# Optimization experiments

Hardware: AMD Instinct MI355X
Metric: run time of the kernel (lower is better)

## Reference

```python
import jax, jax.numpy as jnp
import numpy as np

N, E, F_IN, H, O = 50000, 800000, 128, 64, 1


def _gcn_conv(x, row, col, ew, W, b, n_nodes):
    """PyG GCNConv: add self-loops (weight 1), symmetric deg normalization,
    linear transform (no bias inside lin), scatter-add aggregation, then +bias."""
    loop = jnp.arange(n_nodes, dtype=row.dtype)
    r = jnp.concatenate([row, loop])
    c = jnp.concatenate([col, loop])
    w = jnp.concatenate([ew, jnp.ones((n_nodes,), dtype=ew.dtype)])
    deg = jax.ops.segment_sum(w, c, num_segments=n_nodes)            # [N]
    dis = jnp.where(deg > 0, jax.lax.rsqrt(jnp.maximum(deg, 1e-12)), 0.0)
    norm = dis[r] * w * dis[c]                                       # [E+N]
    h = x @ W                                                        # [N, out]
    msg = h[r] * norm[:, None]                                       # gather + scale
    agg = jax.ops.segment_sum(msg, c, num_segments=n_nodes)          # scatter-add
    return agg + b


def setup_inputs() -> dict:
    key = jax.random.key(0)
    ks = jax.random.split(key, 14)
    s = 0.02
    return {
        "x": jax.random.normal(ks[0], (N, F_IN), dtype=jnp.float32),
        "edge_index": jax.random.randint(ks[1], (2, E), 0, N, dtype=jnp.int64),
        "edge_weight": jax.random.uniform(ks[2], (E,), dtype=jnp.float32),
        "W1": jax.random.normal(ks[3], (F_IN, H), dtype=jnp.float32) * s,
        "b1": jnp.zeros((H,), dtype=jnp.float32),
        "W2": jax.random.normal(ks[4], (H, H), dtype=jnp.float32) * s,
        "b2": jnp.zeros((H,), dtype=jnp.float32),
        "W_ih": jax.random.normal(ks[5], (4 * H, H), dtype=jnp.float32) * s,
        "W_hh": jax.random.normal(ks[6], (4 * H, H), dtype=jnp.float32) * s,
        "b_ih": jax.random.normal(ks[7], (4 * H,), dtype=jnp.float32) * s,
        "b_hh": jax.random.normal(ks[8], (4 * H,), dtype=jnp.float32) * s,
        "W_reg": jax.random.normal(ks[9], (H, O), dtype=jnp.float32) * s,
        "b_reg": jnp.zeros((O,), dtype=jnp.float32),
    }


def reference(x, edge_index, edge_weight, W1, b1, W2, b2,
              W_ih, W_hh, b_ih, b_hh, W_reg, b_reg):
    row, col = edge_index[0], edge_index[1]
    n = x.shape[0]
    h = jax.nn.relu(_gcn_conv(x, row, col, edge_weight, W1, b1, n))
    h = jax.nn.relu(_gcn_conv(h, row, col, edge_weight, W2, b2, n))
    # single-step LSTM, zero initial (h0, c0); PyTorch gate order i, f, g, o
    hd = W_ih.shape[1]
    h0 = jnp.zeros((n, hd), dtype=h.dtype)
    gates = h @ W_ih.T + h0 @ W_hh.T + b_ih + b_hh                   # [N, 4H]
    i, f, g, o = jnp.split(gates, 4, axis=-1)
    c = jax.nn.sigmoid(f) * 0.0 + jax.nn.sigmoid(i) * jnp.tanh(g)    # c0 = 0
    hn = jax.nn.sigmoid(o) * jnp.tanh(c)                             # lstm_out[:, -1]
    return hn @ W_reg + b_reg
```

## Files before the change

kernel.cpp:

```cpp
#include <hip/hip_runtime.h>
#include <math.h>


#define QN 6272
#define NOCT 8
#define NPAD (NOCT * QN)
#define NSLICE 128
#define HIST_BLOCKS (NSLICE * NOCT)

__device__ __forceinline__ float sigmoidf_(float x) {
    return 1.0f / (1.0f + expf(-x));
}

__global__ __launch_bounds__(256) void hist_gemm1_k(
        const int* __restrict__ col, unsigned short* __restrict__ part,
        int E, int N,
        const float* __restrict__ x, const float* __restrict__ W1,
        float* __restrict__ C) {
    extern __shared__ char smem[];
    const int t = threadIdx.x;
    if (blockIdx.x < HIST_BLOCKS) {
        int* hc = (int*)smem;
        const int s = blockIdx.x >> 3;
        const int q = blockIdx.x & 7;
        const int lo = q * QN;
        for (int i = t; i < QN; i += 256) hc[i] = 0;
        __syncthreads();
        const int per = (E + NSLICE - 1) / NSLICE;
        const int e0 = s * per, e1 = min(E, e0 + per);
        int e = e0 + t;
        for (; e + 768 < e1; e += 1024) {
            int c0 = col[e], c1 = col[e + 256], c2 = col[e + 512], c3 = col[e + 768];
            unsigned r0 = (unsigned)(c0 - lo), r1 = (unsigned)(c1 - lo);
            unsigned r2 = (unsigned)(c2 - lo), r3 = (unsigned)(c3 - lo);
            if (r0 < (unsigned)QN && (unsigned)c0 < (unsigned)N) atomicAdd(&hc[r0], 1);
            if (r1 < (unsigned)QN && (unsigned)c1 < (unsigned)N) atomicAdd(&hc[r1], 1);
            if (r2 < (unsigned)QN && (unsigned)c2 < (unsigned)N) atomicAdd(&hc[r2], 1);
            if (r3 < (unsigned)QN && (unsigned)c3 < (unsigned)N) atomicAdd(&hc[r3], 1);
        }
        for (; e < e1; e += 256) {
            int c = col[e];
            unsigned rel = (unsigned)(c - lo);
            if (rel < (unsigned)QN && (unsigned)c < (unsigned)N) atomicAdd(&hc[rel], 1);
        }
        __syncthreads();
        unsigned short* dst = part + (size_t)s * NPAD + lo;
        for (int i = t; i < QN; i += 256) dst[i] = (unsigned short)hc[i];
    } else {
        float (*xs)[68] = (float (*)[68])smem;
        float* ws = (float*)(smem + 64 * 68 * sizeof(float));
        const int n0 = (int)(blockIdx.x - HIST_BLOCKS) * 64;
        for (int base = t * 4; base < 128 * 64; base += 1024)
            *(float4*)(ws + base) = *(const float4*)(W1 + base);
        const int cg = t & 15, ng = t >> 4;
        const int colj = cg * 4, nb = ng * 4;
        float acc[4][4];
#pragma unroll
        for (int i = 0; i < 4; ++i)
#pragma unroll
            for (int j = 0; j < 4; ++j) acc[i][j] = 0.0f;
        for (int k0 = 0; k0 < 128; k0 += 64) {
            __syncthreads();
            for (int base = t * 4; base < 64 * 64; base += 1024) {
                int r = base >> 6, k = base & 63;
                int node = n0 + r;
                float4 v = make_float4(0.f, 0.f, 0.f, 0.f);
                if (node < N) v = *(const float4*)(x + (size_t)node * 128 + k0 + k);
                *(float4*)&xs[r][k] = v;
            }
            __syncthreads();
#pragma unroll 4
            for (int kk = 0; kk < 64; kk += 4) {
                float4 a[4];
#pragma unroll
                for (int i = 0; i < 4; ++i) a[i] = *(float4*)&xs[nb + i][kk];
#pragma unroll
                for (int j = 0; j < 4; ++j) {
                    float4 bv = *(float4*)&ws[(size_t)(k0 + kk + j) * 64 + colj];
                    float av[4];
                    switch (j) {
                        case 0: av[0]=a[0].x; av[1]=a[1].x; av[2]=a[2].x; av[3]=a[3].x; break;
                        case 1: av[0]=a[0].y; av[1]=a[1].y; av[2]=a[2].y; av[3]=a[3].y; break;
                        case 2: av[0]=a[0].z; av[1]=a[1].z; av[2]=a[2].z; av[3]=a[3].z; break;
                        default:av[0]=a[0].w; av[1]=a[1].w; av[2]=a[2].w; av[3]=a[3].w; break;
                    }
#pragma unroll
                    for (int i = 0; i < 4; ++i) {
                        acc[i][0] = fmaf(av[i], bv.x, acc[i][0]);
                        acc[i][1] = fmaf(av[i], bv.y, acc[i][1]);
                        acc[i][2] = fmaf(av[i], bv.z, acc[i][2]);
                        acc[i][3] = fmaf(av[i], bv.w, acc[i][3]);
                    }
                }
            }
        }
#pragma unroll
        for (int i = 0; i < 4; ++i) {
            int node = n0 + nb + i;
            if (node < N)
                *(float4*)(C + (size_t)node * 64 + colj) =
                    make_float4(acc[i][0], acc[i][1], acc[i][2], acc[i][3]);
        }
    }
}

__global__ __launch_bounds__(256) void prefixA_k(const unsigned short* __restrict__ part,
                                                 unsigned short* __restrict__ coff,
                                                 int* __restrict__ cnt,
                                                 int* __restrict__ bsum) {
    __shared__ int r[256];
    const int t = threadIdx.x;
    const int i = blockIdx.x * 256 + t;
    int acc = 0;
    for (int s = 0; s < NSLICE; ++s) {
        size_t idx = (size_t)s * NPAD + i;
        coff[idx] = (unsigned short)acc;
        acc += part[idx];
    }
    cnt[i] = acc;
    r[t] = acc;
    __syncthreads();
#pragma unroll
    for (int off = 128; off > 0; off >>= 1) {
        if (t < off) r[t] += r[t + off];
        __syncthreads();
    }
    if (t == 0) bsum[blockIdx.x] = r[0];
}

__global__ __launch_bounds__(256) void scanBC_k(const int* __restrict__ cnt,
                                                const int* __restrict__ bsum,
                                                int* __restrict__ rowptr, int NBLK) {
    __shared__ int s[2][256];
    __shared__ int red[256];
    const int t = threadIdx.x, b = blockIdx.x;
    const int i = b * 256 + t;
    int v = cnt[i];
    int pin = 0;
    s[0][t] = v;
    __syncthreads();
#pragma unroll
    for (int off = 1; off < 256; off <<= 1) {
        int xo = s[pin][t];
        if (t >= off) xo += s[pin][t - off];
        s[pin ^ 1][t] = xo;
        pin ^= 1;
        __syncthreads();
    }
    int excl = s[pin][t] - v;
    red[t] = (t < b && t < NBLK) ? bsum[t] : 0;
    __syncthreads();
#pragma unroll
    for (int off = 128; off > 0; off >>= 1) {
        if (t < off) red[t] += red[t + off];
        __syncthreads();
    }
    rowptr[i] = excl + red[0];
}

__global__ __launch_bounds__(256) void fill_k(const int* __restrict__ row,
                                              const int* __restrict__ col,
                                              const float* __restrict__ ew,
                                              const int* __restrict__ rowptr,
                                              const unsigned short* __restrict__ coff,
                                              int2* __restrict__ pairs, int E, int N) {
    __shared__ int lcur[QN];
    const int t = threadIdx.x;
    const int s = blockIdx.x >> 3;
    const int q = blockIdx.x & 7;
    const int lo = q * QN;
    const unsigned short* cof = coff + (size_t)s * NPAD + lo;
    const int* rp = rowptr + lo;
    for (int i = t; i < QN; i += 256) lcur[i] = rp[i] + (int)cof[i];
    __syncthreads();
    const int per = (E + NSLICE - 1) / NSLICE;
    const int e0 = s * per, e1 = min(E, e0 + per);
    int e = e0 + t;
    for (; e + 768 < e1; e += 1024) {
        int c0 = col[e], c1 = col[e + 256], c2 = col[e + 512], c3 = col[e + 768];
        unsigned r0 = (unsigned)(c0 - lo), r1 = (unsigned)(c1 - lo);
        unsigned r2 = (unsigned)(c2 - lo), r3 = (unsigned)(c3 - lo);
        if (r0 < (unsigned)QN && (unsigned)c0 < (unsigned)N) {
            int r = row[e]; float w = ew[e];
            if ((unsigned)r >= (unsigned)N) { r = 0; w = 0.0f; }
            pairs[atomicAdd(&lcur[r0], 1)] = make_int2(r, __float_as_int(w));
        }
        if (r1 < (unsigned)QN && (unsigned)c1 < (unsigned)N) {
            int r = row[e + 256]; float w = ew[e + 256];
            if ((unsigned)r >= (unsigned)N) { r = 0; w = 0.0f; }
            pairs[atomicAdd(&lcur[r1], 1)] = make_int2(r, __float_as_int(w));
        }
        if (r2 < (unsigned)QN && (unsigned)c2 < (unsigned)N) {
            int r = row[e + 512]; float w = ew[e + 512];
            if ((unsigned)r >= (unsigned)N) { r = 0; w = 0.0f; }
            pairs[atomicAdd(&lcur[r2], 1)] = make_int2(r, __float_as_int(w));
        }
        if (r3 < (unsigned)QN && (unsigned)c3 < (unsigned)N) {
            int r = row[e + 768]; float w = ew[e + 768];
            if ((unsigned)r >= (unsigned)N) { r = 0; w = 0.0f; }
            pairs[atomicAdd(&lcur[r3], 1)] = make_int2(r, __float_as_int(w));
        }
    }
    for (; e < e1; e += 256) {
        int c = col[e];
        unsigned rel = (unsigned)(c - lo);
        if (rel < (unsigned)QN && (unsigned)c < (unsigned)N) {
            int r = row[e]; float w = ew[e];
            if ((unsigned)r >= (unsigned)N) { r = 0; w = 0.0f; }
            pairs[atomicAdd(&lcur[rel], 1)] = make_int2(r, __float_as_int(w));
        }
    }
}

__global__ __launch_bounds__(256) void degsum_k(const int* __restrict__ rowptr,
                                                const int2* __restrict__ pairs,
                                                float* __restrict__ dis, int N) {
    int i = blockIdx.x * 256 + threadIdx.x;
    if (i >= N) return;
    int b = rowptr[i], en = rowptr[i + 1];
    float s = 0.0f;
    for (int e = b; e < en; ++e) s += __int_as_float(pairs[e].y);
    dis[i] = rsqrtf(s + 1.0f);
}

__global__ __launch_bounds__(256) void aggregate_k(const float* __restrict__ h,
                                                   const int* __restrict__ rowptr,
                                                   const int2* __restrict__ pairs,
                                                   const float* __restrict__ dis,
                                                   const float* __restrict__ bias,
                                                   float* __restrict__ out, int N) {
    const int t = threadIdx.x;
    const int lane = t & 63;
    const int n0 = (blockIdx.x * 4 + (t >> 6)) * 4;
    if (n0 >= N) return;

    int rp[5];
#pragma unroll
    for (int k = 0; k < 5; ++k) rp[k] = rowptr[min(n0 + k, N)];
    const int beg = rp[0], end = rp[4];

    float acc[4] = {0.f, 0.f, 0.f, 0.f};
    for (int base = beg; base < end; base += 64) {
        const int m = min(64, end - base);
        int ps = 0; float pv = 0.0f;
        if (lane < m) {
            int2 p = pairs[base + lane];
            ps = p.x;
            pv = __int_as_float(p.y) * dis[p.x];
        }
        const unsigned pu = __float_as_uint(pv);
#pragma unroll
        for (int i = 0; i < 4; ++i) {
            const int s0 = max(rp[i] - base, 0);
            const int s1 = min(rp[i + 1] - base, m);
            int jj = s0;
            for (; jj + 8 <= s1; jj += 8) {
                int a0 = __builtin_amdgcn_readlane(ps, jj);
                int a1 = __builtin_amdgcn_readlane(ps, jj + 1);
                int a2 = __builtin_amdgcn_readlane(ps, jj + 2);
                int a3 = __builtin_amdgcn_readlane(ps, jj + 3);
                int a4 = __builtin_amdgcn_readlane(ps, jj + 4);
                int a5 = __builtin_amdgcn_readlane(ps, jj + 5);
                int a6 = __builtin_amdgcn_readlane(ps, jj + 6);
                int a7 = __builtin_amdgcn_readlane(ps, jj + 7);
                float v0 = __uint_as_float(__builtin_amdgcn_readlane(pu, jj));
                float v1 = __uint_as_float(__builtin_amdgcn_readlane(pu, jj + 1));
                float v2 = __uint_as_float(__builtin_amdgcn_readlane(pu, jj + 2));
                float v3 = __uint_as_float(__builtin_amdgcn_readlane(pu, jj + 3));
                float v4 = __uint_as_float(__builtin_amdgcn_readlane(pu, jj + 4));
                float v5 = __uint_as_float(__builtin_amdgcn_readlane(pu, jj + 5));
                float v6 = __uint_as_float(__builtin_amdgcn_readlane(pu, jj + 6));
                float v7 = __uint_as_float(__builtin_amdgcn_readlane(pu, jj + 7));
                float h0 = h[(size_t)a0 * 64 + lane];
                float h1 = h[(size_t)a1 * 64 + lane];
                float h2 = h[(size_t)a2 * 64 + lane];
                float h3 = h[(size_t)a3 * 64 + lane];
                float h4 = h[(size_t)a4 * 64 + lane];
                float h5 = h[(size_t)a5 * 64 + lane];
                float h6 = h[(size_t)a6 * 64 + lane];
                float h7 = h[(size_t)a7 * 64 + lane];
                acc[i] = fmaf(h0, v0, acc[i]);
                acc[i] = fmaf(h1, v1, acc[i]);
                acc[i] = fmaf(h2, v2, acc[i]);
                acc[i] = fmaf(h3, v3, acc[i]);
                acc[i] = fmaf(h4, v4, acc[i]);
                acc[i] = fmaf(h5, v5, acc[i]);
                acc[i] = fmaf(h6, v6, acc[i]);
                acc[i] = fmaf(h7, v7, acc[i]);
            }
            for (; jj + 4 <= s1; jj += 4) {
                int a0 = __builtin_amdgcn_readlane(ps, jj);
                int a1 = __builtin_amdgcn_readlane(ps, jj + 1);
                int a2 = __builtin_amdgcn_readlane(ps, jj + 2);
                int a3 = __builtin_amdgcn_readlane(ps, jj + 3);
                float v0 = __uint_as_float(__builtin_amdgcn_readlane(pu, jj));
                float v1 = __uint_as_float(__builtin_amdgcn_readlane(pu, jj + 1));
                float v2 = __uint_as_float(__builtin_amdgcn_readlane(pu, jj + 2));
                float v3 = __uint_as_float(__builtin_amdgcn_readlane(pu, jj + 3));
                float h0 = h[(size_t)a0 * 64 + lane];
                float h1 = h[(size_t)a1 * 64 + lane];
                float h2 = h[(size_t)a2 * 64 + lane];
                float h3 = h[(size_t)a3 * 64 + lane];
                acc[i] = fmaf(h0, v0, acc[i]);
                acc[i] = fmaf(h1, v1, acc[i]);
                acc[i] = fmaf(h2, v2, acc[i]);
                acc[i] = fmaf(h3, v3, acc[i]);
            }
            for (; jj < s1; ++jj) {
                int   a0 = __builtin_amdgcn_readlane(ps, jj);
                float v0 = __uint_as_float(__builtin_amdgcn_readlane(pu, jj));
                acc[i] = fmaf(h[(size_t)a0 * 64 + lane], v0, acc[i]);
            }
        }
    }
#pragma unroll
    for (int i = 0; i < 4; ++i) {
        int node = n0 + i;
        if (node < N) {
            float d = dis[node];
            float a = acc[i];
            a = fmaf(d, h[(size_t)node * 64 + lane], a);
            a = fmaf(d, a, bias[lane]);
            out[(size_t)node * 64 + lane] = fmaxf(a, 0.0f);
        }
    }
}

template <int K>
__global__ __launch_bounds__(256) void gemm64_k(const float* __restrict__ A,
                                                const float* __restrict__ W,
                                                float* __restrict__ C, int M) {
    __shared__ float xs[64][68];
    __shared__ float ws[K][64];
    const int t  = threadIdx.x;
    const int n0 = blockIdx.x * 64;

    for (int base = t * 4; base < K * 64; base += 1024)
        *(float4*)((float*)ws + base) = *(const float4*)(W + base);

    const int cg = t & 15, ng = t >> 4;
    const int col = cg * 4, nb = ng * 4;
    float acc[4][4];
#pragma unroll
    for (int i = 0; i < 4; ++i)
#pragma unroll
        for (int j = 0; j < 4; ++j) acc[i][j] = 0.0f;

    for (int k0 = 0; k0 < K; k0 += 64) {
        __syncthreads();
        for (int base = t * 4; base < 64 * 64; base += 1024) {
            int r = base >> 6, k = base & 63;
            int node = n0 + r;
            float4 v = make_float4(0.f, 0.f, 0.f, 0.f);
            if (node < M) v = *(const float4*)(A + (size_t)node * K + k0 + k);
            *(float4*)&xs[r][k] = v;
        }
        __syncthreads();
#pragma unroll 4
        for (int kk = 0; kk < 64; kk += 4) {
            float4 a[4];
#pragma unroll
            for (int i = 0; i < 4; ++i) a[i] = *(float4*)&xs[nb + i][kk];
#pragma unroll
            for (int j = 0; j < 4; ++j) {
                float4 bv = *(float4*)&ws[k0 + kk + j][col];
                float av[4];
                switch (j) {
                    case 0: av[0]=a[0].x; av[1]=a[1].x; av[2]=a[2].x; av[3]=a[3].x; break;
                    case 1: av[0]=a[0].y; av[1]=a[1].y; av[2]=a[2].y; av[3]=a[3].y; break;
                    case 2: av[0]=a[0].z; av[1]=a[1].z; av[2]=a[2].z; av[3]=a[3].z; break;
                    default:av[0]=a[0].w; av[1]=a[1].w; av[2]=a[2].w; av[3]=a[3].w; break;
                }
#pragma unroll
                for (int i = 0; i < 4; ++i) {
                    acc[i][0] = fmaf(av[i], bv.x, acc[i][0]);
                    acc[i][1] = fmaf(av[i], bv.y, acc[i][1]);
                    acc[i][2] = fmaf(av[i], bv.z, acc[i][2]);
                    acc[i][3] = fmaf(av[i], bv.w, acc[i][3]);
                }
            }
        }
    }
#pragma unroll
    for (int i = 0; i < 4; ++i) {
        int node = n0 + nb + i;
        if (node < M)
            *(float4*)(C + (size_t)node * 64 + col) =
                make_float4(acc[i][0], acc[i][1], acc[i][2], acc[i][3]);
    }
}

__global__ __launch_bounds__(256) void lstm_head_k(const float* __restrict__ h,
                                                   const float* __restrict__ Wih,
                                                   const float* __restrict__ bih,
                                                   const float* __restrict__ bhh,
                                                   const float* __restrict__ Wreg,
                                                   const float* __restrict__ breg,
                                                   float* __restrict__ out, int N) {
    __shared__ float wt[64 * 192];
    __shared__ float hsT[64 * 64];
    const int t = threadIdx.x;
    const int n0 = blockIdx.x * 64;

    {
        const int j = t & 63, kq = (t >> 6) * 4;
#pragma unroll
        for (int gid = 0; gid < 3; ++gid) {
            const int gBase = (gid == 0) ? 0 : (gid == 1 ? 128 : 192);
            const int gOff = gid * 64;
#pragma unroll
            for (int it = 0; it < 4; ++it) {
                int k0 = it * 16 + kq;
                float4 w = *(const float4*)(Wih + (size_t)(gBase + j) * 64 + k0);
                wt[(k0 + 0) * 192 + gOff + j] = w.x;
                wt[(k0 + 1) * 192 + gOff + j] = w.y;
                wt[(k0 + 2) * 192 + gOff + j] = w.z;
                wt[(k0 + 3) * 192 + gOff + j] = w.w;
            }
        }
    }
    {
        const int r = t & 63, kq = (t >> 6) * 4;
        const int node = n0 + r;
#pragma unroll
        for (int it = 0; it < 4; ++it) {
            int k0 = it * 16 + kq;
            float4 v = make_float4(0.f, 0.f, 0.f, 0.f);
            if (node < N) v = *(const float4*)(h + (size_t)node * 64 + k0);
            hsT[(k0 + 0) * 64 + r] = v.x;
            hsT[(k0 + 1) * 64 + r] = v.y;
            hsT[(k0 + 2) * 64 + r] = v.z;
            hsT[(k0 + 3) * 64 + r] = v.w;
        }
    }

    const int cg = t & 15, ng = t >> 4;
    const int col = cg * 4, nb = ng * 4;
    float4 bi4 = *(const float4*)(bih + col);
    float4 bg4 = *(const float4*)(bih + 128 + col);
    float4 bo4 = *(const float4*)(bih + 192 + col);
    {
        float4 h0 = *(const float4*)(bhh + col);
        float4 h1 = *(const float4*)(bhh + 128 + col);
        float4 h2 = *(const float4*)(bhh + 192 + col);
        bi4.x += h0.x; bi4.y += h0.y; bi4.z += h0.z; bi4.w += h0.w;
        bg4.x += h1.x; bg4.y += h1.y; bg4.z += h1.z; bg4.w += h1.w;
        bo4.x += h2.x; bo4.y += h2.y; bo4.z += h2.z; bo4.w += h2.w;
    }
    float4 wr4 = *(const float4*)(Wreg + col);
    const float br = breg[0];

    __syncthreads();

    float ai[4][4], ag[4][4], ao[4][4];
#pragma unroll
    for (int i = 0; i < 4; ++i)
#pragma unroll
        for (int j = 0; j < 4; ++j) { ai[i][j] = 0.f; ag[i][j] = 0.f; ao[i][j] = 0.f; }

#pragma unroll 4
    for (int k = 0; k < 64; ++k) {
        float4 a  = *(float4*)&hsT[k * 64 + nb];
        float4 wi = *(float4*)&wt[k * 192 + col];
        float4 wg = *(float4*)&wt[k * 192 + 64 + col];
        float4 wo = *(float4*)&wt[k * 192 + 128 + col];
        const float av[4] = {a.x, a.y, a.z, a.w};
#pragma unroll
        for (int i = 0; i < 4; ++i) {
            ai[i][0] = fmaf(av[i], wi.x, ai[i][0]);
            ai[i][1] = fmaf(av[i], wi.y, ai[i][1]);
            ai[i][2] = fmaf(av[i], wi.z, ai[i][2]);
            ai[i][3] = fmaf(av[i], wi.w, ai[i][3]);
            ag[i][0] = fmaf(av[i], wg.x, ag[i][0]);
            ag[i][1] = fmaf(av[i], wg.y, ag[i][1]);
            ag[i][2] = fmaf(av[i], wg.z, ag[i][2]);
            ag[i][3] = fmaf(av[i], wg.w, ag[i][3]);
            ao[i][0] = fmaf(av[i], wo.x, ao[i][0]);
            ao[i][1] = fmaf(av[i], wo.y, ao[i][1]);
            ao[i][2] = fmaf(av[i], wo.z, ao[i][2]);
            ao[i][3] = fmaf(av[i], wo.w, ao[i][3]);
        }
    }

    const float bia[4] = {bi4.x, bi4.y, bi4.z, bi4.w};
    const float bga[4] = {bg4.x, bg4.y, bg4.z, bg4.w};
    const float boa[4] = {bo4.x, bo4.y, bo4.z, bo4.w};
    const float wra[4] = {wr4.x, wr4.y, wr4.z, wr4.w};
    float res[4];
#pragma unroll
    for (int i = 0; i < 4; ++i) {
        float s = 0.f;
#pragma unroll
        for (int j = 0; j < 4; ++j) {
            float gi = ai[i][j] + bia[j];
            float gg = ag[i][j] + bga[j];
            float go = ao[i][j] + boa[j];
            float cc = sigmoidf_(gi) * tanhf(gg);
            float hn = sigmoidf_(go) * tanhf(cc);
            s = fmaf(hn, wra[j], s);
        }
        res[i] = s;
    }
#pragma unroll
    for (int off = 8; off > 0; off >>= 1) {
#pragma unroll
        for (int i = 0; i < 4; ++i) res[i] += __shfl_down(res[i], off);
    }
    if (cg == 0) {
#pragma unroll
        for (int i = 0; i < 4; ++i) {
            int node = n0 + nb + i;
            if (node < N) out[node] = res[i] + br;
        }
    }
}

extern "C" void kernel_launch(void* const* d_in, const int* in_sizes, int n_in,
                              void* d_out, int out_size, void* d_ws, size_t ws_size,
                              hipStream_t stream) {
    const float* x    = (const float*)d_in[0];
    const int*   ei   = (const int*)d_in[1];
    const float* ew   = (const float*)d_in[2];
    const float* W1   = (const float*)d_in[3];
    const float* b1   = (const float*)d_in[4];
    const float* W2   = (const float*)d_in[5];
    const float* b2   = (const float*)d_in[6];
    const float* Wih  = (const float*)d_in[7];
    const float* bih  = (const float*)d_in[9];
    const float* bhh  = (const float*)d_in[10];
    const float* Wreg = (const float*)d_in[11];
    const float* breg = (const float*)d_in[12];
    float* out = (float*)d_out;

    const int N = out_size;
    const int E = in_sizes[1] / 2;
    const int* row = ei;
    const int* col = ei + E;

    const int NB   = (N + 255) / 256;
    const int NBLK = NPAD / 256;

    char* wsb = (char*)d_ws;
    size_t off = 0;
    unsigned short* part = (unsigned short*)(wsb + off); off += (size_t)NSLICE * NPAD * 2;
    unsigned short* coff = (unsigned short*)(wsb + off); off += (size_t)NSLICE * NPAD * 2;
    float* bufA   = (float*)(wsb + off); off += (size_t)N * 64 * 4;
    float* bufB   = (float*)(wsb + off); off += (size_t)N * 64 * 4;
    float* bufC   = (float*)(wsb + off); off += (size_t)N * 64 * 4;
    int2*  pairs  = (int2*) (wsb + off); off += (size_t)E * 8;
    float* dis    = (float*)(wsb + off); off += (size_t)NPAD * 4;
    int*   cnt    = (int*)  (wsb + off); off += (size_t)NPAD * 4;
    int*   rowptr = (int*)  (wsb + off); off += ((size_t)NPAD + 64) * 4;
    int*   bsum   = (int*)  (wsb + off); off += 1024;

    const int gb = (N + 63) / 64;
    const int ab = (N + 15) / 16;
    const size_t DSM = 64 * 68 * sizeof(float) + 128 * 64 * sizeof(float);

    hist_gemm1_k<<<HIST_BLOCKS + gb, 256, DSM, stream>>>(col, part, E, N, x, W1, bufA);
    prefixA_k<<<NBLK, 256, 0, stream>>>(part, coff, cnt, bsum);
    scanBC_k<<<NBLK, 256, 0, stream>>>(cnt, bsum, rowptr, NBLK);
    fill_k<<<HIST_BLOCKS, 256, 0, stream>>>(row, col, ew, rowptr, coff, pairs, E, N);
    degsum_k<<<NB, 256, 0, stream>>>(rowptr, pairs, dis, N);
    aggregate_k<<<ab, 256, 0, stream>>>(bufA, rowptr, pairs, dis, b1, bufB, N);
    gemm64_k<64><<<gb, 256, 0, stream>>>(bufB, W2, bufC, N);
    aggregate_k<<<ab, 256, 0, stream>>>(bufC, rowptr, pairs, dis, b2, bufA, N);
    lstm_head_k<<<gb, 256, 0, stream>>>(bufA, Wih, bih, bhh, Wreg, breg, out, N);
}
```

Baseline: 269.3 us.

## Fuse first-layer aggregation with the second-layer W2 GEMM

The first GCN aggregation is combined with the following 64x64 linear transform in a single kernel. Each block gathers 16 nodes, writes the ReLU'd rows to shared memory, then multiplies them by W2 held in shared memory. This removes one kernel launch and the write and re-read of an N×64 intermediate buffer. In exchange every block reloads W2 into LDS and adds a barrier, and the early return for out-of-range waves is dropped.

```diff
diff --git a/kernel.cpp b/kernel.cpp
--- a/kernel.cpp
+++ b/kernel.cpp
@@ -223,23 +223,11 @@
     dis[i] = rsqrtf(s + 1.0f);
 }
 
-__global__ __launch_bounds__(256) void aggregate_k(const float* __restrict__ h,
-                                                   const int* __restrict__ rowptr,
-                                                   const int2* __restrict__ pairs,
-                                                   const float* __restrict__ dis,
-                                                   const float* __restrict__ bias,
-                                                   float* __restrict__ out, int N) {
-    const int t = threadIdx.x;
-    const int lane = t & 63;
-    const int n0 = (blockIdx.x * 4 + (t >> 6)) * 4;
-    if (n0 >= N) return;
-
-    int rp[5];
-#pragma unroll
-    for (int k = 0; k < 5; ++k) rp[k] = rowptr[min(n0 + k, N)];
+__device__ __forceinline__ void gather4(const float* __restrict__ h,
+                                        const int2* __restrict__ pairs,
+                                        const float* __restrict__ dis,
+                                        const int* rp, int lane, float acc[4]) {
     const int beg = rp[0], end = rp[4];
-
-    float acc[4] = {0.f, 0.f, 0.f, 0.f};
     for (int base = beg; base < end; base += 64) {
         const int m = min(64, end - base);
         int ps = 0; float pv = 0.0f;
@@ -313,6 +301,26 @@
             }
         }
     }
+}
+
+__global__ __launch_bounds__(256) void aggregate_k(const float* __restrict__ h,
+                                                   const int* __restrict__ rowptr,
+                                                   const int2* __restrict__ pairs,
+                                                   const float* __restrict__ dis,
+                                                   const float* __restrict__ bias,
+                                                   float* __restrict__ out, int N) {
+    const int t = threadIdx.x;
+    const int lane = t & 63;
+    const int n0 = (blockIdx.x * 4 + (t >> 6)) * 4;
+    if (n0 >= N) return;
+
+    int rp[5];
+#pragma unroll
+    for (int k = 0; k < 5; ++k) rp[k] = rowptr[min(n0 + k, N)];
+
+    float acc[4] = {0.f, 0.f, 0.f, 0.f};
+    gather4(h, pairs, dis, rp, lane, acc);
+
 #pragma unroll
     for (int i = 0; i < 4; ++i) {
         int node = n0 + i;
@@ -326,68 +334,57 @@
     }
 }
 
-template <int K>
-__global__ __launch_bounds__(256) void gemm64_k(const float* __restrict__ A,
-                                                const float* __restrict__ W,
-                                                float* __restrict__ C, int M) {
-    __shared__ float xs[64][68];
-    __shared__ float ws[K][64];
-    const int t  = threadIdx.x;
-    const int n0 = blockIdx.x * 64;
-
-    for (int base = t * 4; base < K * 64; base += 1024)
-        *(float4*)((float*)ws + base) = *(const float4*)(W + base);
-
-    const int cg = t & 15, ng = t >> 4;
-    const int col = cg * 4, nb = ng * 4;
-    float acc[4][4];
-#pragma unroll
-    for (int i = 0; i < 4; ++i)
-#pragma unroll
-        for (int j = 0; j < 4; ++j) acc[i][j] = 0.0f;
-
-    for (int k0 = 0; k0 < K; k0 += 64) {
-        __syncthreads();
-        for (int base = t * 4; base < 64 * 64; base += 1024) {
-            int r = base >> 6, k = base & 63;
-            int node = n0 + r;
-            float4 v = make_float4(0.f, 0.f, 0.f, 0.f);
-            if (node < M) v = *(const float4*)(A + (size_t)node * K + k0 + k);
-            *(float4*)&xs[r][k] = v;
-        }
-        __syncthreads();
-#pragma unroll 4
-        for (int kk = 0; kk < 64; kk += 4) {
-            float4 a[4];
-#pragma unroll
-            for (int i = 0; i < 4; ++i) a[i] = *(float4*)&xs[nb + i][kk];
-#pragma unroll
-            for (int j = 0; j < 4; ++j) {
-                float4 bv = *(float4*)&ws[k0 + kk + j][col];
-                float av[4];
-                switch (j) {
-                    case 0: av[0]=a[0].x; av[1]=a[1].x; av[2]=a[2].x; av[3]=a[3].x; break;
-                    case 1: av[0]=a[0].y; av[1]=a[1].y; av[2]=a[2].y; av[3]=a[3].y; break;
-                    case 2: av[0]=a[0].z; av[1]=a[1].z; av[2]=a[2].z; av[3]=a[3].z; break;
-                    default:av[0]=a[0].w; av[1]=a[1].w; av[2]=a[2].w; av[3]=a[3].w; break;
-                }
-#pragma unroll
-                for (int i = 0; i < 4; ++i) {
-                    acc[i][0] = fmaf(av[i], bv.x, acc[i][0]);
-                    acc[i][1] = fmaf(av[i], bv.y, acc[i][1]);
-                    acc[i][2] = fmaf(av[i], bv.z, acc[i][2]);
-                    acc[i][3] = fmaf(av[i], bv.w, acc[i][3]);
-                }
-            }
-        }
-    }
+__global__ __launch_bounds__(256) void agg_gemm_k(const float* __restrict__ h,
+                                                  const int* __restrict__ rowptr,
+                                                  const int2* __restrict__ pairs,
+                                                  const float* __restrict__ dis,
+                                                  const float* __restrict__ bias,
+                                                  const float* __restrict__ W2,
+                                                  float* __restrict__ outC, int N) {
+    __shared__ float w2s[64 * 64];
+    __shared__ float tile[16][66];
+    const int t = threadIdx.x;
+    const int lane = t & 63, w = t >> 6;
+    const int n0 = blockIdx.x * 16 + w * 4;
+
+    for (int base = t * 4; base < 64 * 64; base += 1024)
+        *(float4*)(w2s + base) = *(const float4*)(W2 + base);
+
+    int rp[5];
+#pragma unroll
+    for (int k = 0; k < 5; ++k) rp[k] = rowptr[min(min(n0 + k, N), N)];
+
+    float acc[4] = {0.f, 0.f, 0.f, 0.f};
+    gather4(h, pairs, dis, rp, lane, acc);
+
 #pragma unroll
     for (int i = 0; i < 4; ++i) {
-        int node = n0 + nb + i;
-        if (node < M)
-            *(float4*)(C + (size_t)node * 64 + col) =
-                make_float4(acc[i][0], acc[i][1], acc[i][2], acc[i][3]);
-    }
+        int node = n0 + i;
+        float a = 0.0f;
+        if (node < N) {
+            float d = dis[node];
+            a = acc[i];
+            a = fmaf(d, h[(size_t)node * 64 + lane], a);
+            a = fmaf(d, a, bias[lane]);
+            a = fmaxf(a, 0.0f);
+        }
+        tile[w * 4 + i][lane] = a;
+    }
+    __syncthreads();
+
+    const int n = t >> 4, oc = (t & 15) * 4;
+    float4 o = make_float4(0.f, 0.f, 0.f, 0.f);
+#pragma unroll 8
+    for (int f = 0; f < 64; ++f) {
+        float a = tile[n][f];
+        float4 wv = *(float4*)&w2s[f * 64 + oc];
+        o.x = fmaf(a, wv.x, o.x);
+        o.y = fmaf(a, wv.y, o.y);
+        o.z = fmaf(a, wv.z, o.z);
+        o.w = fmaf(a, wv.w, o.w);
+    }
+    const int node = blockIdx.x * 16 + n;
+    if (node < N) *(float4*)(outC + (size_t)node * 64 + oc) = o;
 }
 
 __global__ __launch_bounds__(256) void lstm_head_k(const float* __restrict__ h,
@@ -545,7 +542,6 @@
     unsigned short* part = (unsigned short*)(wsb + off); off += (size_t)NSLICE * NPAD * 2;
     unsigned short* coff = (unsigned short*)(wsb + off); off += (size_t)NSLICE * NPAD * 2;
     float* bufA   = (float*)(wsb + off); off += (size_t)N * 64 * 4;
-    float* bufB   = (float*)(wsb + off); off += (size_t)N * 64 * 4;
     float* bufC   = (float*)(wsb + off); off += (size_t)N * 64 * 4;
     int2*  pairs  = (int2*) (wsb + off); off += (size_t)E * 8;
     float* dis    = (float*)(wsb + off); off += (size_t)NPAD * 4;
@@ -562,8 +558,7 @@
     scanBC_k<<<NBLK, 256, 0, stream>>>(cnt, bsum, rowptr, NBLK);
     fill_k<<<HIST_BLOCKS, 256, 0, stream>>>(row, col, ew, rowptr, coff, pairs, E, N);
     degsum_k<<<NB, 256, 0, stream>>>(rowptr, pairs, dis, N);
-    aggregate_k<<<ab, 256, 0, stream>>>(bufA, rowptr, pairs, dis, b1, bufB, N);
-    gemm64_k<64><<<gb, 256, 0, stream>>>(bufB, W2, bufC, N);
+    agg_gemm_k<<<ab, 256, 0, stream>>>(bufA, rowptr, pairs, dis, b1, W2, bufC, N);
     aggregate_k<<<ab, 256, 0, stream>>>(bufC, rowptr, pairs, dis, b2, bufA, N);
     lstm_head_k<<<gb, 256, 0, stream>>>(bufA, Wih, bih, bhh, Wreg, breg, out, N);
 }
```

Result: no change. 265.7 us (-1.3%).
